# Optimization experiments

Measured on AMD Instinct MI355X. Metric: run time of the kernel, lower is better.

Reference implementation:

```python
import jax, jax.numpy as jnp
from jax import lax
import numpy as np

B, P, M1, M2, M3 = 128, 168, 2, 2, 2
M = M1 * M2 * M3
HIDC, HIDR, HIDS, CK, SKIP, HW = 50, 50, 5, 6, 24, 24
PT = (P - CK) // SKIP  # int((P-Ck)/skip) = 6
L = P - CK + 1         # 163


def gru(xs, w_ih, w_hh, b_ih, b_hh, hid):
    # xs: [T, N, in]; torch nn.GRU cell semantics, h0 = 0. Returns final h: [N, hid].
    def step(h, x):
        gi = x @ w_ih.T + b_ih
        gh = h @ w_hh.T + b_hh
        ir, iz, inn = jnp.split(gi, 3, axis=-1)
        hr, hz, hn = jnp.split(gh, 3, axis=-1)
        r = jax.nn.sigmoid(ir + hr)
        z = jax.nn.sigmoid(iz + hz)
        n = jnp.tanh(inn + r * hn)
        return (1.0 - z) * n + z * h, None
    h0 = jnp.zeros((xs.shape[1], hid), xs.dtype)
    h, _ = lax.scan(step, h0, xs)
    return h


def setup_inputs() -> dict:
    key = jax.random.key(0)
    ks = jax.random.split(key, 16)
    O = P * HIDC * CK  # 50400 conv output channels
    d = {
        'x': jax.random.normal(ks[0], (B, P, M1, M2, M3), jnp.float32),
        'conv_w': jax.random.normal(ks[1], (O, P, M1, M2, M3), jnp.float32) * 0.02,
        'conv_b': jax.random.normal(ks[2], (O,), jnp.float32) * 0.02,
        'g1_wih': jax.random.normal(ks[3], (3 * HIDR, HIDC), jnp.float32) * 0.1,
        'g1_whh': jax.random.normal(ks[4], (3 * HIDR, HIDR), jnp.float32) * 0.1,
        'g1_bih': jax.random.normal(ks[5], (3 * HIDR,), jnp.float32) * 0.1,
        'g1_bhh': jax.random.normal(ks[6], (3 * HIDR,), jnp.float32) * 0.1,
        'gs_wih': jax.random.normal(ks[7], (3 * HIDS, HIDC), jnp.float32) * 0.1,
        'gs_whh': jax.random.normal(ks[8], (3 * HIDS, HIDS), jnp.float32) * 0.1,
        'gs_bih': jax.random.normal(ks[9], (3 * HIDS,), jnp.float32) * 0.1,
        'gs_bhh': jax.random.normal(ks[10], (3 * HIDS,), jnp.float32) * 0.1,
        'l1_w': jax.random.normal(ks[11], (M, HIDR + SKIP * HIDS), jnp.float32) * 0.1,
        'l1_b': jax.random.normal(ks[12], (M,), jnp.float32) * 0.1,
        'hw_w': jax.random.normal(ks[13], (1, HW), jnp.float32) * 0.1,
        'hw_b': jax.random.normal(ks[14], (1,), jnp.float32) * 0.1,
    }
    return d


def reference(x, conv_w, conv_b, g1_wih, g1_whh, g1_bih, g1_bhh,
              gs_wih, gs_whh, gs_bih, gs_bhh, l1_w, l1_b, hw_w, hw_b):
    # Conv3d with kernel == full spatial extent is a dense matmul over (P*m1*m2*m3).
    xf = x.reshape(B, -1)                       # [B, P*M]
    wf = conv_w.reshape(conv_w.shape[0], -1)    # [O, P*M]
    c = jax.nn.relu(xf @ wf.T + conv_b)         # [B, O]
    c = c.reshape(B, HIDC, CK, P)
    # Diagonal strided sum (the torch triple loop): res1[b,c,t] = sum_k c[b,c,k,k+t]
    res1 = sum(c[:, :, k, k:k + L] for k in range(CK))  # [B, HIDC, L]
    # dropout: eval mode (identity)
    r = gru(jnp.transpose(res1, (2, 0, 1)), g1_wih, g1_whh, g1_bih, g1_bhh, HIDR)  # [B, HIDR]
    # skip GRU
    s = res1[:, :, -PT * SKIP:]                          # [B, HIDC, PT*SKIP]
    s = s.reshape(B, HIDC, PT, SKIP)
    s = jnp.transpose(s, (2, 0, 3, 1)).reshape(PT, B * SKIP, HIDC)
    hs = gru(s, gs_wih, gs_whh, gs_bih, gs_bhh, HIDS)    # [B*SKIP, HIDS]
    hs = hs.reshape(B, SKIP * HIDS)
    r = jnp.concatenate([r, hs], axis=1)                 # [B, HIDR + SKIP*HIDS]
    res = r @ l1_w.T + l1_b                              # [B, M]
    # highway (AR) component over the last HW timesteps
    z = x[:, -HW:].reshape(B, HW, M)                     # [B, HW, M]
    z = jnp.transpose(z, (0, 2, 1)).reshape(-1, HW)      # [B*M, HW]
    z = z @ hw_w.T + hw_b                                # [B*M, 1]
    res = res + z.reshape(B, M)
    res = jax.nn.sigmoid(res)
    return res.reshape(B, M1, M2, M3)
```

## Files before the change

### kernel.cpp

```cpp
#include <hip/hip_runtime.h>
#include <hip/hip_bf16.h>
#include <cstdint>


typedef __attribute__((ext_vector_type(8))) short short8;
typedef __attribute__((ext_vector_type(4))) float f32x4;

__device__ __forceinline__ unsigned short bf16rn(float f) {
    unsigned u = __float_as_uint(f);
    return (unsigned short)((u + 0x7FFFu + ((u >> 16) & 1u)) >> 16);
}
__device__ __forceinline__ unsigned pk2(float a, float b) {
    return ((unsigned)bf16rn(b) << 16) | (unsigned)bf16rn(a);
}
__device__ __forceinline__ uint4 pack8(float4 f0, float4 f1) {
    uint4 u;
    u.x = pk2(f0.x, f0.y); u.y = pk2(f0.z, f0.w);
    u.z = pk2(f1.x, f1.y); u.w = pk2(f1.z, f1.w);
    return u;
}
__device__ __forceinline__ float bf2f(unsigned short u) {
    return __uint_as_float((unsigned)u << 16);
}
__device__ __forceinline__ float sigmf(float x) { return 1.f / (1.f + __expf(-x)); }
__device__ __forceinline__ float tanhf_(float x) { return 1.f - 2.f / (__expf(2.f * x) + 1.f); }

__global__ __launch_bounds__(256, 2)
void k1_conv_gemm(const float* __restrict__ x, const float* __restrict__ w,
                  const float* __restrict__ bias, unsigned short* __restrict__ c) {
    __shared__ uint4 a_lds[8 * 129];
    __shared__ uint4 b_lds[8 * 113];
    const int tid  = threadIdx.x;
    const int n0   = blockIdx.x * 112;
    const int wave = tid >> 6, lane = tid & 63;
    const int quad = lane >> 4, m16 = lane & 15;

    f32x4 acc[2][7];
#pragma unroll
    for (int i = 0; i < 2; ++i)
#pragma unroll
        for (int j = 0; j < 7; ++j) acc[i][j] = (f32x4){0.f, 0.f, 0.f, 0.f};

    float4 pa[4][2];
    float4 pb[4][2];

    auto issue = [&](int kb) {
#pragma unroll
        for (int i = 0; i < 4; ++i) {
            int row = (tid >> 3) + 32 * i;
            const float* gp = x + row * 1344 + kb + (tid & 7) * 8;
            pa[i][0] = *reinterpret_cast<const float4*>(gp);
            pa[i][1] = *reinterpret_cast<const float4*>(gp + 4);
        }
#pragma unroll
        for (int i = 0; i < 4; ++i) {
            int idx = tid + 256 * i;
            if (idx < 896) {
                int row = idx >> 3;
                const float* gp = w + (size_t)(n0 + row) * 1344 + kb + (idx & 7) * 8;
                pb[i][0] = *reinterpret_cast<const float4*>(gp);
                pb[i][1] = *reinterpret_cast<const float4*>(gp + 4);
            }
        }
    };

    issue(0);
    for (int kb = 0; kb < 1344; kb += 64) {
#pragma unroll
        for (int i = 0; i < 4; ++i) {
            int idx = tid + 256 * i;
            int row = idx >> 3, ks = idx & 7;
            a_lds[ks * 129 + row] = pack8(pa[i][0], pa[i][1]);
        }
#pragma unroll
        for (int i = 0; i < 4; ++i) {
            int idx = tid + 256 * i;
            if (idx < 896) {
                int row = idx >> 3, ks = idx & 7;
                b_lds[ks * 113 + row] = pack8(pb[i][0], pb[i][1]);
            }
        }
        __syncthreads();
        if (kb + 64 < 1344) issue(kb + 64);
#pragma unroll
        for (int half = 0; half < 2; ++half) {
            const int kp = half * 4 + quad;
            short8 af[2], bfr[7];
#pragma unroll
            for (int rt = 0; rt < 2; ++rt)
                af[rt] = ((const short8*)a_lds)[kp * 129 + wave * 32 + rt * 16 + m16];
#pragma unroll
            for (int ct = 0; ct < 7; ++ct)
                bfr[ct] = ((const short8*)b_lds)[kp * 113 + ct * 16 + m16];
#pragma unroll
            for (int rt = 0; rt < 2; ++rt)
#pragma unroll
                for (int ct = 0; ct < 7; ++ct)
                    acc[rt][ct] = __builtin_amdgcn_mfma_f32_16x16x32_bf16(
                        af[rt], bfr[ct], acc[rt][ct], 0, 0, 0);
        }
        __syncthreads();
    }
#pragma unroll
    for (int ct = 0; ct < 7; ++ct) {
        int col = n0 + ct * 16 + m16;
        float bv = bias[col];
#pragma unroll
        for (int rt = 0; rt < 2; ++rt) {
#pragma unroll
            for (int r = 0; r < 4; ++r) {
                int grow = wave * 32 + rt * 16 + quad * 4 + r;
                float v = acc[rt][ct][r] + bv;
                v = fmaxf(v, 0.f);
                c[(size_t)grow * 50400 + col] = bf16rn(v);
            }
        }
    }
}

__global__ __launch_bounds__(256)
void k2_diag(const unsigned short* __restrict__ c, float* __restrict__ res1) {
    __shared__ float rloc[50 * 164];
    const int b = blockIdx.x;
    const unsigned short* cb = c + (size_t)b * 50400;
    for (int idx = threadIdx.x; idx < 8150; idx += 256) {
        int hc = idx / 163, t = idx - hc * 163;
        int base = hc * 1008 + t;
        float s = 0.f;
#pragma unroll
        for (int k = 0; k < 6; ++k) s += bf2f(cb[base + 169 * k]);
        rloc[hc * 164 + t] = s;
    }
    __syncthreads();
    for (int idx = threadIdx.x; idx < 8150; idx += 256) {
        int t = idx / 50, hc = idx - t * 50;
        res1[(size_t)(t * 128 + b) * 50 + hc] = rloc[hc * 164 + t];
    }
}

__global__ __launch_bounds__(256)
void k3_gi1(const float* __restrict__ res1, const float* __restrict__ wih,
            const float* __restrict__ bih, float* __restrict__ gi1) {
    __shared__ float wl[150 * 52];
    __shared__ float xl[64 * 52];
    const int row0 = blockIdx.x * 64;
    for (int idx = threadIdx.x; idx < 7500; idx += 256) {
        int r = idx / 50, j = idx - r * 50;
        wl[r * 52 + j] = wih[idx];
    }
    for (int idx = threadIdx.x; idx < 3200; idx += 256) {
        int r = idx / 50, j = idx - r * 50;
        xl[r * 52 + j] = res1[(size_t)row0 * 50 + idx];
    }
    __syncthreads();
    for (int e = threadIdx.x; e < 9600; e += 256) {
        int rr = e / 150, cc = e - rr * 150;
        float4 a0 = {0.f, 0.f, 0.f, 0.f};
        const float* xp = &xl[rr * 52];
        const float* wp = &wl[cc * 52];
#pragma unroll
        for (int j = 0; j < 48; j += 4) {
            float4 xv = *reinterpret_cast<const float4*>(xp + j);
            float4 wv = *reinterpret_cast<const float4*>(wp + j);
            a0.x += xv.x * wv.x; a0.y += xv.y * wv.y;
            a0.z += xv.z * wv.z; a0.w += xv.w * wv.w;
        }
        float acc = bih[cc] + xp[48] * wp[48] + xp[49] * wp[49]
                  + (a0.x + a0.y) + (a0.z + a0.w);
        gi1[(size_t)(row0 + rr) * 150 + cc] = acc;
    }
}

__global__ __launch_bounds__(256)
void k3_gi2(const float* __restrict__ res1, const float* __restrict__ wih,
            const float* __restrict__ bih, float* __restrict__ gi2) {
    __shared__ float wl[15 * 52];
    __shared__ float xl[64 * 52];
    const int row0 = blockIdx.x * 64;
    for (int idx = threadIdx.x; idx < 750; idx += 256) {
        int r = idx / 50, j = idx - r * 50;
        wl[r * 52 + j] = wih[idx];
    }
    for (int idx = threadIdx.x; idx < 3200; idx += 256) {
        int rr = idx / 50, j = idx - rr * 50;
        int r = row0 + rr;
        int pt = r / 3072, bsk = r - pt * 3072;
        int b = bsk / 24, sk = bsk - b * 24;
        int t = 19 + pt * 24 + sk;
        xl[rr * 52 + j] = res1[(size_t)(t * 128 + b) * 50 + j];
    }
    __syncthreads();
    for (int e = threadIdx.x; e < 960; e += 256) {
        int rr = e / 15, cc = e - rr * 15;
        float4 a0 = {0.f, 0.f, 0.f, 0.f};
        const float* xp = &xl[rr * 52];
        const float* wp = &wl[cc * 52];
#pragma unroll
        for (int j = 0; j < 48; j += 4) {
            float4 xv = *reinterpret_cast<const float4*>(xp + j);
            float4 wv = *reinterpret_cast<const float4*>(wp + j);
            a0.x += xv.x * wv.x; a0.y += xv.y * wv.y;
            a0.z += xv.z * wv.z; a0.w += xv.w * wv.w;
        }
        float acc = bih[cc] + xp[48] * wp[48] + xp[49] * wp[49]
                  + (a0.x + a0.y) + (a0.z + a0.w);
        gi2[(size_t)(row0 + rr) * 15 + cc] = acc;
    }
}

__global__ __launch_bounds__(64)
void k4_gru1(const float* __restrict__ gi1, const float* __restrict__ whh,
             const float* __restrict__ bhh, float* __restrict__ r1) {
    __shared__ float wl[7500];
    __shared__ __align__(16) float hl[2][64];
    const int b = blockIdx.x;
    const int l = threadIdx.x;
    for (int idx = l; idx < 7500; idx += 64) wl[idx] = whh[idx];
    hl[0][l] = 0.f;
    hl[1][l] = 0.f;
    __syncthreads();
    const int lc = (l < 50) ? l : 49;
    float wr[50], wz[50], wn[50];
#pragma unroll
    for (int j = 0; j < 50; ++j) {
        wr[j] = wl[lc * 50 + j];
        wz[j] = wl[(50 + lc) * 50 + j];
        wn[j] = wl[(100 + lc) * 50 + j];
    }
    const float bhr = bhh[lc], bhz = bhh[50 + lc], bhn = bhh[100 + lc];
    float hcur = 0.f;
    const float* gp = gi1 + (size_t)b * 150;
    float gir = gp[lc], giz = gp[50 + lc], gin = gp[100 + lc];
    int p = 0;
    for (int t = 0; t < 163; ++t) {
        float ngir = 0.f, ngiz = 0.f, ngin = 0.f;
        if (t < 162) {
            const float* gq = gp + 150 * 128;
            ngir = gq[lc]; ngiz = gq[50 + lc]; ngin = gq[100 + lc];
        }
        const float* hp = hl[p];
        float ar = bhr, az = bhz, an = bhn;
#pragma unroll
        for (int j4 = 0; j4 < 12; ++j4) {
            float4 hv = *reinterpret_cast<const float4*>(hp + 4 * j4);
            ar += wr[4 * j4 + 0] * hv.x + wr[4 * j4 + 1] * hv.y +
                  wr[4 * j4 + 2] * hv.z + wr[4 * j4 + 3] * hv.w;
            az += wz[4 * j4 + 0] * hv.x + wz[4 * j4 + 1] * hv.y +
                  wz[4 * j4 + 2] * hv.z + wz[4 * j4 + 3] * hv.w;
            an += wn[4 * j4 + 0] * hv.x + wn[4 * j4 + 1] * hv.y +
                  wn[4 * j4 + 2] * hv.z + wn[4 * j4 + 3] * hv.w;
        }
        {
            float h48 = hp[48], h49 = hp[49];
            ar += wr[48] * h48 + wr[49] * h49;
            az += wz[48] * h48 + wz[49] * h49;
            an += wn[48] * h48 + wn[49] * h49;
        }
        float rg = sigmf(gir + ar);
        float zg = sigmf(giz + az);
        float ng = tanhf_(gin + rg * an);
        float hn = (1.f - zg) * ng + zg * hcur;
        hl[1 - p][l] = hn;
        __syncthreads();
        p ^= 1;
        hcur = hn;
        gir = ngir; giz = ngiz; gin = ngin;
        gp += 150 * 128;
    }
    if (l < 50) r1[b * 50 + l] = hcur;
}

__global__ __launch_bounds__(256)
void k5_gru2(const float* __restrict__ gi2, const float* __restrict__ whh,
             const float* __restrict__ bhh, float* __restrict__ hs) {
    __shared__ float wl[75];
    __shared__ float bl[15];
    const int tid = threadIdx.x;
    if (tid < 75) wl[tid] = whh[tid];
    if (tid < 15) bl[tid] = bhh[tid];
    __syncthreads();
    const int bsk = blockIdx.x * 256 + tid;
    float h[5] = {0.f, 0.f, 0.f, 0.f, 0.f};
    for (int pt = 0; pt < 6; ++pt) {
        const float* gp = gi2 + (size_t)(pt * 3072 + bsk) * 15;
        float gi[15];
#pragma unroll
        for (int i = 0; i < 15; ++i) gi[i] = gp[i];
        float gh[15];
#pragma unroll
        for (int i = 0; i < 15; ++i) {
            float s = bl[i];
#pragma unroll
            for (int j = 0; j < 5; ++j) s += wl[i * 5 + j] * h[j];
            gh[i] = s;
        }
#pragma unroll
        for (int u = 0; u < 5; ++u) {
            float rg = sigmf(gi[u] + gh[u]);
            float zg = sigmf(gi[5 + u] + gh[5 + u]);
            float ng = tanhf_(gi[10 + u] + rg * gh[10 + u]);
            h[u] = (1.f - zg) * ng + zg * h[u];
        }
    }
#pragma unroll
    for (int u = 0; u < 5; ++u) hs[bsk * 5 + u] = h[u];
}

__global__ __launch_bounds__(256)
void k6_final(const float* __restrict__ r1, const float* __restrict__ hs,
              const float* __restrict__ l1w, const float* __restrict__ l1b,
              const float* __restrict__ x, const float* __restrict__ hww,
              const float* __restrict__ hwb, float* __restrict__ out) {
    const int tid = blockIdx.x * 256 + threadIdx.x;
    if (tid >= 1024) return;
    const int b = tid >> 3, m = tid & 7;
    float acc = l1b[m];
    const float* wrow = l1w + m * 170;
    const float* rb = r1 + b * 50;
#pragma unroll
    for (int j = 0; j < 50; ++j) acc += rb[j] * wrow[j];
    const float* hb = hs + b * 120;
#pragma unroll
    for (int j = 0; j < 120; ++j) acc += hb[j] * wrow[50 + j];
    float z = hwb[0];
    const float* xb = x + b * 1344 + 144 * 8 + m;
#pragma unroll
    for (int wi = 0; wi < 24; ++wi) z += xb[wi * 8] * hww[wi];
    out[tid] = 1.f / (1.f + __expf(-(acc + z)));
}

extern "C" void kernel_launch(void* const* d_in, const int* in_sizes, int n_in,
                              void* d_out, int out_size, void* d_ws, size_t ws_size,
                              hipStream_t stream) {
    const float* x      = (const float*)d_in[0];
    const float* conv_w = (const float*)d_in[1];
    const float* conv_b = (const float*)d_in[2];
    const float* g1_wih = (const float*)d_in[3];
    const float* g1_whh = (const float*)d_in[4];
    const float* g1_bih = (const float*)d_in[5];
    const float* g1_bhh = (const float*)d_in[6];
    const float* gs_wih = (const float*)d_in[7];
    const float* gs_whh = (const float*)d_in[8];
    const float* gs_bih = (const float*)d_in[9];
    const float* gs_bhh = (const float*)d_in[10];
    const float* l1_w   = (const float*)d_in[11];
    const float* l1_b   = (const float*)d_in[12];
    const float* hw_w   = (const float*)d_in[13];
    const float* hw_b   = (const float*)d_in[14];
    float* out = (float*)d_out;

    char* ws = (char*)d_ws;
    unsigned short* c   = (unsigned short*)(ws);
    float* res1         = (float*)(ws + 12902400);
    float* gi1          = (float*)(ws + 17075200);
    float* gi2          = (float*)(ws + 29593600);
    float* r1           = (float*)(ws + 30699520);
    float* hs           = (float*)(ws + 30725120);

    hipLaunchKernelGGL(k1_conv_gemm, dim3(450), dim3(256), 0, stream, x, conv_w, conv_b, c);
    hipLaunchKernelGGL(k2_diag,      dim3(128), dim3(256), 0, stream, c, res1);
    hipLaunchKernelGGL(k3_gi1,       dim3(326), dim3(256), 0, stream, res1, g1_wih, g1_bih, gi1);
    hipLaunchKernelGGL(k3_gi2,       dim3(288), dim3(256), 0, stream, res1, gs_wih, gs_bih, gi2);
    hipLaunchKernelGGL(k4_gru1,      dim3(128), dim3(64),  0, stream, gi1, g1_whh, g1_bhh, r1);
    hipLaunchKernelGGL(k5_gru2,      dim3(12),  dim3(256), 0, stream, gi2, gs_whh, gs_bhh, hs);
    hipLaunchKernelGGL(k6_final,     dim3(4),   dim3(256), 0, stream, r1, hs, l1_w, l1_b, x, hw_w, hw_b, out);
}
```

Measured before the change: 589.8 us.

## Fuse diagonal sum, GRU input projections, both GRUs and output head into one kernel

Replaces the diagonal-sum, two input-projection, two GRU and final head kernels with a single per-batch kernel of 384 threads. Intermediates (res1, gi1, gi2, r1, hs) stay in shared memory instead of round-tripping through global workspace, and the skip GRU runs on a second wave alongside the main recurrence. This removes five launches and the global writes and reads of the large gi1 buffer. In exchange the serial recurrence now synchronises all six waves every step, the input projections read weights straight from global memory, and the large LDS footprint allows only one block per CU.

```diff
diff --git a/kernel.cpp b/kernel.cpp
--- a/kernel.cpp
+++ b/kernel.cpp
@@ -118,12 +118,29 @@
     }
 }
 
-__global__ __launch_bounds__(256)
-void k2_diag(const unsigned short* __restrict__ c, float* __restrict__ res1) {
+__global__ __launch_bounds__(384, 1)
+void k_fused(const unsigned short* __restrict__ c,
+             const float* __restrict__ g1_wih, const float* __restrict__ g1_whh,
+             const float* __restrict__ g1_bih, const float* __restrict__ g1_bhh,
+             const float* __restrict__ gs_wih, const float* __restrict__ gs_whh,
+             const float* __restrict__ gs_bih, const float* __restrict__ gs_bhh,
+             const float* __restrict__ l1_w, const float* __restrict__ l1_b,
+             const float* __restrict__ x, const float* __restrict__ hw_w,
+             const float* __restrict__ hw_b, float* __restrict__ out) {
     __shared__ float rloc[50 * 164];
-    const int b = blockIdx.x;
+    __shared__ float gi1l[163 * 150];
+    __shared__ float gi2l[144 * 15];
+    __shared__ float l1wl[8 * 170];
+    __shared__ __align__(16) float hl[2][64];
+    __shared__ float hsl[120];
+    __shared__ float r1l[64];
+
+    const int b    = blockIdx.x;
+    const int tid  = threadIdx.x;
+    const int wave = tid >> 6, lane = tid & 63;
+
     const unsigned short* cb = c + (size_t)b * 50400;
-    for (int idx = threadIdx.x; idx < 8150; idx += 256) {
+    for (int idx = tid; idx < 8150; idx += 384) {
         int hc = idx / 163, t = idx - hc * 163;
         int base = hc * 1008 + t;
         float s = 0.f;
@@ -131,202 +148,138 @@
         for (int k = 0; k < 6; ++k) s += bf2f(cb[base + 169 * k]);
         rloc[hc * 164 + t] = s;
     }
+    for (int idx = tid; idx < 1360; idx += 384) l1wl[idx] = l1_w[idx];
     __syncthreads();
-    for (int idx = threadIdx.x; idx < 8150; idx += 256) {
-        int t = idx / 50, hc = idx - t * 50;
-        res1[(size_t)(t * 128 + b) * 50 + hc] = rloc[hc * 164 + t];
-    }
-}
-
-__global__ __launch_bounds__(256)
-void k3_gi1(const float* __restrict__ res1, const float* __restrict__ wih,
-            const float* __restrict__ bih, float* __restrict__ gi1) {
-    __shared__ float wl[150 * 52];
-    __shared__ float xl[64 * 52];
-    const int row0 = blockIdx.x * 64;
-    for (int idx = threadIdx.x; idx < 7500; idx += 256) {
-        int r = idx / 50, j = idx - r * 50;
-        wl[r * 52 + j] = wih[idx];
-    }
-    for (int idx = threadIdx.x; idx < 3200; idx += 256) {
-        int r = idx / 50, j = idx - r * 50;
-        xl[r * 52 + j] = res1[(size_t)row0 * 50 + idx];
+
+    {
+        const int tB   = (wave >> 1) * 64 + lane;
+        const int half = wave & 1;
+        if (tB < 163) {
+            float xcol[50];
+#pragma unroll
+            for (int j = 0; j < 50; ++j) xcol[j] = rloc[j * 164 + tB];
+
+            const int c0 = __builtin_amdgcn_readfirstlane(half * 75);
+            const float* wbase = g1_wih + c0 * 50;
+            float* gdst = &gi1l[tB * 150 + c0];
+            for (int cc = 0; cc < 75; ++cc) {
+                const float* wp = wbase + cc * 50;
+                float acc = g1_bih[c0 + cc];
+#pragma unroll
+                for (int j = 0; j < 50; ++j) acc += xcol[j] * wp[j];
+                gdst[cc] = acc;
+            }
+            if (tB >= 19) {
+                const int r2 = tB - 19;
+                const int d0 = __builtin_amdgcn_readfirstlane(half * 8);
+                const int ncol = half ? 7 : 8;
+                float* g2 = &gi2l[r2 * 15];
+                for (int cc = 0; cc < ncol; ++cc) {
+                    const float* wp = gs_wih + (d0 + cc) * 50;
+                    float acc = gs_bih[d0 + cc];
+#pragma unroll
+                    for (int j = 0; j < 50; ++j) acc += xcol[j] * wp[j];
+                    g2[d0 + cc] = acc;
+                }
+            }
+        }
     }
     __syncthreads();
-    for (int e = threadIdx.x; e < 9600; e += 256) {
-        int rr = e / 150, cc = e - rr * 150;
-        float4 a0 = {0.f, 0.f, 0.f, 0.f};
-        const float* xp = &xl[rr * 52];
-        const float* wp = &wl[cc * 52];
-#pragma unroll
-        for (int j = 0; j < 48; j += 4) {
-            float4 xv = *reinterpret_cast<const float4*>(xp + j);
-            float4 wv = *reinterpret_cast<const float4*>(wp + j);
-            a0.x += xv.x * wv.x; a0.y += xv.y * wv.y;
-            a0.z += xv.z * wv.z; a0.w += xv.w * wv.w;
-        }
-        float acc = bih[cc] + xp[48] * wp[48] + xp[49] * wp[49]
-                  + (a0.x + a0.y) + (a0.z + a0.w);
-        gi1[(size_t)(row0 + rr) * 150 + cc] = acc;
-    }
-}
-
-__global__ __launch_bounds__(256)
-void k3_gi2(const float* __restrict__ res1, const float* __restrict__ wih,
-            const float* __restrict__ bih, float* __restrict__ gi2) {
-    __shared__ float wl[15 * 52];
-    __shared__ float xl[64 * 52];
-    const int row0 = blockIdx.x * 64;
-    for (int idx = threadIdx.x; idx < 750; idx += 256) {
-        int r = idx / 50, j = idx - r * 50;
-        wl[r * 52 + j] = wih[idx];
-    }
-    for (int idx = threadIdx.x; idx < 3200; idx += 256) {
-        int rr = idx / 50, j = idx - rr * 50;
-        int r = row0 + rr;
-        int pt = r / 3072, bsk = r - pt * 3072;
-        int b = bsk / 24, sk = bsk - b * 24;
-        int t = 19 + pt * 24 + sk;
-        xl[rr * 52 + j] = res1[(size_t)(t * 128 + b) * 50 + j];
-    }
-    __syncthreads();
-    for (int e = threadIdx.x; e < 960; e += 256) {
-        int rr = e / 15, cc = e - rr * 15;
-        float4 a0 = {0.f, 0.f, 0.f, 0.f};
-        const float* xp = &xl[rr * 52];
-        const float* wp = &wl[cc * 52];
-#pragma unroll
-        for (int j = 0; j < 48; j += 4) {
-            float4 xv = *reinterpret_cast<const float4*>(xp + j);
-            float4 wv = *reinterpret_cast<const float4*>(wp + j);
-            a0.x += xv.x * wv.x; a0.y += xv.y * wv.y;
-            a0.z += xv.z * wv.z; a0.w += xv.w * wv.w;
-        }
-        float acc = bih[cc] + xp[48] * wp[48] + xp[49] * wp[49]
-                  + (a0.x + a0.y) + (a0.z + a0.w);
-        gi2[(size_t)(row0 + rr) * 15 + cc] = acc;
-    }
-}
-
-__global__ __launch_bounds__(64)
-void k4_gru1(const float* __restrict__ gi1, const float* __restrict__ whh,
-             const float* __restrict__ bhh, float* __restrict__ r1) {
-    __shared__ float wl[7500];
-    __shared__ __align__(16) float hl[2][64];
-    const int b = blockIdx.x;
-    const int l = threadIdx.x;
-    for (int idx = l; idx < 7500; idx += 64) wl[idx] = whh[idx];
-    hl[0][l] = 0.f;
-    hl[1][l] = 0.f;
-    __syncthreads();
-    const int lc = (l < 50) ? l : 49;
+
     float wr[50], wz[50], wn[50];
-#pragma unroll
-    for (int j = 0; j < 50; ++j) {
-        wr[j] = wl[lc * 50 + j];
-        wz[j] = wl[(50 + lc) * 50 + j];
-        wn[j] = wl[(100 + lc) * 50 + j];
-    }
-    const float bhr = bhh[lc], bhz = bhh[50 + lc], bhn = bhh[100 + lc];
-    float hcur = 0.f;
-    const float* gp = gi1 + (size_t)b * 150;
-    float gir = gp[lc], giz = gp[50 + lc], gin = gp[100 + lc];
+    float bhr = 0.f, bhz = 0.f, bhn = 0.f, hcur = 0.f;
+    int lc = 0;
+    float* wl1 = rloc;
+    if (wave == 0) {
+        for (int idx = lane; idx < 7500; idx += 64) wl1[idx] = g1_whh[idx];
+        hl[0][lane] = 0.f;
+        hl[1][lane] = 0.f;
+        lc = (lane < 50) ? lane : 49;
+#pragma unroll
+        for (int j = 0; j < 50; ++j) {
+            wr[j] = wl1[lc * 50 + j];
+            wz[j] = wl1[(50 + lc) * 50 + j];
+            wn[j] = wl1[(100 + lc) * 50 + j];
+        }
+        bhr = g1_bhh[lc]; bhz = g1_bhh[50 + lc]; bhn = g1_bhh[100 + lc];
+    }
+    float h2[5] = {0.f, 0.f, 0.f, 0.f, 0.f};
+
     int p = 0;
     for (int t = 0; t < 163; ++t) {
-        float ngir = 0.f, ngiz = 0.f, ngin = 0.f;
-        if (t < 162) {
-            const float* gq = gp + 150 * 128;
-            ngir = gq[lc]; ngiz = gq[50 + lc]; ngin = gq[100 + lc];
-        }
-        const float* hp = hl[p];
-        float ar = bhr, az = bhz, an = bhn;
-#pragma unroll
-        for (int j4 = 0; j4 < 12; ++j4) {
-            float4 hv = *reinterpret_cast<const float4*>(hp + 4 * j4);
-            ar += wr[4 * j4 + 0] * hv.x + wr[4 * j4 + 1] * hv.y +
-                  wr[4 * j4 + 2] * hv.z + wr[4 * j4 + 3] * hv.w;
-            az += wz[4 * j4 + 0] * hv.x + wz[4 * j4 + 1] * hv.y +
-                  wz[4 * j4 + 2] * hv.z + wz[4 * j4 + 3] * hv.w;
-            an += wn[4 * j4 + 0] * hv.x + wn[4 * j4 + 1] * hv.y +
-                  wn[4 * j4 + 2] * hv.z + wn[4 * j4 + 3] * hv.w;
-        }
-        {
-            float h48 = hp[48], h49 = hp[49];
-            ar += wr[48] * h48 + wr[49] * h49;
-            az += wz[48] * h48 + wz[49] * h49;
-            an += wn[48] * h48 + wn[49] * h49;
-        }
-        float rg = sigmf(gir + ar);
-        float zg = sigmf(giz + az);
-        float ng = tanhf_(gin + rg * an);
-        float hn = (1.f - zg) * ng + zg * hcur;
-        hl[1 - p][l] = hn;
+        if (wave == 0) {
+            float gir = gi1l[t * 150 + lc];
+            float giz = gi1l[t * 150 + 50 + lc];
+            float gin = gi1l[t * 150 + 100 + lc];
+            const float* hp = hl[p];
+            float ar = bhr, az = bhz, an = bhn;
+#pragma unroll
+            for (int j4 = 0; j4 < 12; ++j4) {
+                float4 hv = *reinterpret_cast<const float4*>(hp + 4 * j4);
+                ar += wr[4 * j4 + 0] * hv.x + wr[4 * j4 + 1] * hv.y +
+                      wr[4 * j4 + 2] * hv.z + wr[4 * j4 + 3] * hv.w;
+                az += wz[4 * j4 + 0] * hv.x + wz[4 * j4 + 1] * hv.y +
+                      wz[4 * j4 + 2] * hv.z + wz[4 * j4 + 3] * hv.w;
+                an += wn[4 * j4 + 0] * hv.x + wn[4 * j4 + 1] * hv.y +
+                      wn[4 * j4 + 2] * hv.z + wn[4 * j4 + 3] * hv.w;
+            }
+            {
+                float h48 = hp[48], h49 = hp[49];
+                ar += wr[48] * h48 + wr[49] * h49;
+                az += wz[48] * h48 + wz[49] * h49;
+                an += wn[48] * h48 + wn[49] * h49;
+            }
+            float rg = sigmf(gir + ar);
+            float zg = sigmf(giz + az);
+            float ng = tanhf_(gin + rg * an);
+            float hn = (1.f - zg) * ng + zg * hcur;
+            hl[1 - p][lane] = hn;
+            hcur = hn;
+        } else if (wave == 1 && t < 6 && lane < 24) {
+            const float* gp = &gi2l[(t * 24 + lane) * 15];
+            float gi[15];
+#pragma unroll
+            for (int i = 0; i < 15; ++i) gi[i] = gp[i];
+            float gh[15];
+#pragma unroll
+            for (int i = 0; i < 15; ++i) {
+                float s = gs_bhh[i];
+#pragma unroll
+                for (int j = 0; j < 5; ++j) s += gs_whh[i * 5 + j] * h2[j];
+                gh[i] = s;
+            }
+#pragma unroll
+            for (int u = 0; u < 5; ++u) {
+                float rg = sigmf(gi[u] + gh[u]);
+                float zg = sigmf(gi[5 + u] + gh[5 + u]);
+                float ng = tanhf_(gi[10 + u] + rg * gh[10 + u]);
+                h2[u] = (1.f - zg) * ng + zg * h2[u];
+            }
+        }
         __syncthreads();
         p ^= 1;
-        hcur = hn;
-        gir = ngir; giz = ngiz; gin = ngin;
-        gp += 150 * 128;
-    }
-    if (l < 50) r1[b * 50 + l] = hcur;
-}
-
-__global__ __launch_bounds__(256)
-void k5_gru2(const float* __restrict__ gi2, const float* __restrict__ whh,
-             const float* __restrict__ bhh, float* __restrict__ hs) {
-    __shared__ float wl[75];
-    __shared__ float bl[15];
-    const int tid = threadIdx.x;
-    if (tid < 75) wl[tid] = whh[tid];
-    if (tid < 15) bl[tid] = bhh[tid];
+    }
+    if (wave == 0 && lane < 50) r1l[lane] = hcur;
+    if (wave == 1 && lane < 24) {
+#pragma unroll
+        for (int u = 0; u < 5; ++u) hsl[lane * 5 + u] = h2[u];
+    }
     __syncthreads();
-    const int bsk = blockIdx.x * 256 + tid;
-    float h[5] = {0.f, 0.f, 0.f, 0.f, 0.f};
-    for (int pt = 0; pt < 6; ++pt) {
-        const float* gp = gi2 + (size_t)(pt * 3072 + bsk) * 15;
-        float gi[15];
-#pragma unroll
-        for (int i = 0; i < 15; ++i) gi[i] = gp[i];
-        float gh[15];
-#pragma unroll
-        for (int i = 0; i < 15; ++i) {
-            float s = bl[i];
-#pragma unroll
-            for (int j = 0; j < 5; ++j) s += wl[i * 5 + j] * h[j];
-            gh[i] = s;
-        }
-#pragma unroll
-        for (int u = 0; u < 5; ++u) {
-            float rg = sigmf(gi[u] + gh[u]);
-            float zg = sigmf(gi[5 + u] + gh[5 + u]);
-            float ng = tanhf_(gi[10 + u] + rg * gh[10 + u]);
-            h[u] = (1.f - zg) * ng + zg * h[u];
-        }
-    }
-#pragma unroll
-    for (int u = 0; u < 5; ++u) hs[bsk * 5 + u] = h[u];
-}
-
-__global__ __launch_bounds__(256)
-void k6_final(const float* __restrict__ r1, const float* __restrict__ hs,
-              const float* __restrict__ l1w, const float* __restrict__ l1b,
-              const float* __restrict__ x, const float* __restrict__ hww,
-              const float* __restrict__ hwb, float* __restrict__ out) {
-    const int tid = blockIdx.x * 256 + threadIdx.x;
-    if (tid >= 1024) return;
-    const int b = tid >> 3, m = tid & 7;
-    float acc = l1b[m];
-    const float* wrow = l1w + m * 170;
-    const float* rb = r1 + b * 50;
-#pragma unroll
-    for (int j = 0; j < 50; ++j) acc += rb[j] * wrow[j];
-    const float* hb = hs + b * 120;
-#pragma unroll
-    for (int j = 0; j < 120; ++j) acc += hb[j] * wrow[50 + j];
-    float z = hwb[0];
-    const float* xb = x + b * 1344 + 144 * 8 + m;
-#pragma unroll
-    for (int wi = 0; wi < 24; ++wi) z += xb[wi * 8] * hww[wi];
-    out[tid] = 1.f / (1.f + __expf(-(acc + z)));
+
+    if (tid < 8) {
+        const int m = tid;
+        float acc = l1_b[m];
+        const float* wrow = &l1wl[m * 170];
+#pragma unroll
+        for (int j = 0; j < 50; ++j) acc += r1l[j] * wrow[j];
+#pragma unroll
+        for (int j = 0; j < 120; ++j) acc += hsl[j] * wrow[50 + j];
+        float z = hw_b[0];
+        const float* xb = x + (size_t)b * 1344 + 144 * 8 + m;
+#pragma unroll
+        for (int wi = 0; wi < 24; ++wi) z += xb[wi * 8] * hw_w[wi];
+        out[b * 8 + m] = 1.f / (1.f + __expf(-(acc + z)));
+    }
 }
 
 extern "C" void kernel_launch(void* const* d_in, const int* in_sizes, int n_in,
@@ -349,19 +302,11 @@
     const float* hw_b   = (const float*)d_in[14];
     float* out = (float*)d_out;
 
-    char* ws = (char*)d_ws;
-    unsigned short* c   = (unsigned short*)(ws);
-    float* res1         = (float*)(ws + 12902400);
-    float* gi1          = (float*)(ws + 17075200);
-    float* gi2          = (float*)(ws + 29593600);
-    float* r1           = (float*)(ws + 30699520);
-    float* hs           = (float*)(ws + 30725120);
+    unsigned short* c = (unsigned short*)d_ws;
 
     hipLaunchKernelGGL(k1_conv_gemm, dim3(450), dim3(256), 0, stream, x, conv_w, conv_b, c);
-    hipLaunchKernelGGL(k2_diag,      dim3(128), dim3(256), 0, stream, c, res1);
-    hipLaunchKernelGGL(k3_gi1,       dim3(326), dim3(256), 0, stream, res1, g1_wih, g1_bih, gi1);
-    hipLaunchKernelGGL(k3_gi2,       dim3(288), dim3(256), 0, stream, res1, gs_wih, gs_bih, gi2);
-    hipLaunchKernelGGL(k4_gru1,      dim3(128), dim3(64),  0, stream, gi1, g1_whh, g1_bhh, r1);
-    hipLaunchKernelGGL(k5_gru2,      dim3(12),  dim3(256), 0, stream, gi2, gs_whh, gs_bhh, hs);
-    hipLaunchKernelGGL(k6_final,     dim3(4),   dim3(256), 0, stream, r1, hs, l1_w, l1_b, x, hw_w, hw_b, out);
-}
+    hipLaunchKernelGGL(k_fused,      dim3(128), dim3(384), 0, stream,
+                       c, g1_wih, g1_whh, g1_bih, g1_bhh,
+                       gs_wih, gs_whh, gs_bih, gs_bhh,
+                       l1_w, l1_b, x, hw_w, hw_b, out);
+}
```

Result: faster. 566.5 us (-4.0%).
